# Optimization experiments

Hardware: AMD Instinct MI355X
Metric: run time of the kernel (lower is better)

The kernel has to match this reference:

```python
import jax, jax.numpy as jnp
import numpy as np


def setup_inputs() -> dict:
    key = jax.random.key(0)
    k1, k2, k3, k4, k5 = jax.random.split(key, 5)
    B, S, IN, OUT, GS = 64, 1, 8192, 28672, 128
    n_groups = IN // GS  # 64
    return {
        "input": jax.random.normal(k1, (B, S, IN), dtype=jnp.float32),
        # packed int4 weights: two 4-bit values per byte along in_features
        "qweight": jax.random.randint(k2, (IN // 2, OUT), 0, 256, dtype=jnp.int32),
        # per-group scales (small positive, typical of quantized weights)
        "scales": (jax.random.uniform(k3, (n_groups, OUT), dtype=jnp.float32) * 0.01 + 1e-3),
        # per-group zero points, 4-bit range
        "qzeros": jax.random.randint(k4, (n_groups, OUT), 0, 16, dtype=jnp.int32),
        "bias": jax.random.normal(k5, (OUT,), dtype=jnp.float32),
        "group_size": GS,
    }


def _dequant_int4(qweight, scales, qzeros, group_size):
    # qweight: [in/2, out] bytes; low nibble = even k, high nibble = odd k
    half_in, out_f = qweight.shape
    in_f = half_in * 2
    lo = qweight & 0xF
    hi = (qweight >> 4) & 0xF
    # interleave nibbles along in_features -> [in, out]
    w_q = jnp.stack([lo, hi], axis=1).reshape(in_f, out_f).astype(scales.dtype)
    n_groups = scales.shape[0]
    # (q - zero) * scale, per group of `group_size` rows
    w = (w_q.reshape(n_groups, group_size, out_f)
         - qzeros.astype(scales.dtype)[:, None, :]) * scales[:, None, :]
    return w.reshape(in_f, out_f)


def reference(input, qweight, scales, qzeros, bias, group_size):
    # Fused dequant-int4 matmul (decode path, seq_len == 1): y = x @ W + b
    w = _dequant_int4(qweight, scales, qzeros, group_size)  # [in, out]
    return jnp.einsum('bsi,io->bso', input, w) + bias
```

## Files before the change

### kernel.cpp

```cpp
#include <hip/hip_runtime.h>
#include <hip/hip_bf16.h>


typedef float  f32x4 __attribute__((ext_vector_type(4)));
typedef short  s16x8 __attribute__((ext_vector_type(8)));
typedef int    i32x4 __attribute__((ext_vector_type(4)));

#define K_DIM  8192
#define N_DIM  28672
#define BN     64
#define CK     128
#define NCHUNK 64

__device__ s16x8 g_wsa[NCHUNK * 1024];

__device__ f32x4 llvm_amdgcn_raw_buffer_load_v4f32(i32x4 srsrc, int voff, int soff, int aux) __asm("llvm.amdgcn.raw.buffer.load.v4f32");

static __device__ __forceinline__ short f2bf(float f) {
    return (short)__builtin_bit_cast(unsigned short, __float2bfloat16(f));
}
static __device__ __forceinline__ i32x4 make_srsrc(const void* p, unsigned bytes) {
    union { struct { const void* ptr; unsigned rec; unsigned cfg; } s; i32x4 v; } u;
    u.s.ptr = p; u.s.rec = bytes; u.s.cfg = 0x00020000;
    return u.v;
}

__global__ __launch_bounds__(256)
void prep_a_kernel(const float* __restrict__ x) {
    const int tid = threadIdx.x;
    const int c   = blockIdx.x >> 2;
    const int mb  = blockIdx.x & 3;
    const int k8  = tid & 15;
    const int m   = mb * 16 + (tid >> 4);
    const float* src = x + (size_t)m * K_DIM + c * CK + k8 * 8;
    f32x4 a = *(const f32x4*)src;
    f32x4 b = *(const f32x4*)(src + 4);
    s16x8 o;
    o[0] = f2bf(a[0]); o[1] = f2bf(a[1]); o[2] = f2bf(a[2]); o[3] = f2bf(a[3]);
    o[4] = f2bf(b[0]); o[5] = f2bf(b[1]); o[6] = f2bf(b[2]); o[7] = f2bf(b[3]);
    g_wsa[(size_t)c * 1024 + k8 * 64 + m] = o;
}

__global__ __launch_bounds__(512, 4)
void int4gemm_kernel(const int*   __restrict__ qw,
                     const float* __restrict__ sc,
                     const int*   __restrict__ qz,
                     const float* __restrict__ bias,
                     float*       __restrict__ out)
{
    __shared__ s16x8 lB[2][16 * 64];

    const int tid   = threadIdx.x;
    const int lane  = tid & 63;
    const int w     = tid >> 6;
    const int nbase = blockIdx.x * BN;

    const int col  = lane;
    const int*   qcol = qw + nbase + col;
    const float* scol = sc + nbase + col;
    const int*   zcol = qz + nbase + col;

    const int l15 = lane & 15;
    const int lk  = lane >> 4;
    const int mh  = w >> 2;
    const int wn  = (w & 3) * 16;

    const i32x4 srA  = make_srsrc((const void*)g_wsa, NCHUNK * 1024 * 16);
    const int   voffA = (lk * 64 + mh * 32 + l15) * 16;

    f32x4 acc[2];
    acc[0] = (f32x4)0.0f;
    acc[1] = (f32x4)0.0f;

    int   bvC[8], bvB[8], bvN[8];
    float sC, sB_, sN_;
    int   zC, zB_, zN_;

#pragma unroll
    for (int u = 0; u < 8; ++u) {
        bvC[u] = qcol[(size_t)(8 * w + u) * N_DIM];
        bvB[u] = qcol[(size_t)(64 + 8 * w + u) * N_DIM];
    }
    sC  = scol[0];               zC  = zcol[0];
    sB_ = scol[N_DIM];           zB_ = zcol[N_DIM];

#pragma unroll 2
    for (int c = 0; c < NCHUNK; ++c) {
        f32x4 af[8];
#pragma unroll
        for (int ks = 0; ks < 4; ++ks)
#pragma unroll
            for (int mi = 0; mi < 2; ++mi)
                af[ks * 2 + mi] = llvm_amdgcn_raw_buffer_load_v4f32(
                    srA, voffA + mi * 256, c * 16384 + ks * 4096, 0);
        __builtin_amdgcn_sched_barrier(0);

        const int cb = (c + 2) & (NCHUNK - 1);
#pragma unroll
        for (int u = 0; u < 8; ++u)
            bvN[u] = qcol[(size_t)(cb * 64 + 8 * w + u) * N_DIM];
        sN_ = scol[(size_t)cb * N_DIM];
        zN_ = zcol[(size_t)cb * N_DIM];
        __builtin_amdgcn_sched_barrier(0);

        const float s = sC;
        const float o = -(float)zC * s;
        s16x8 c0, c1;
#pragma unroll
        for (int uu = 0; uu < 4; ++uu) {
            const int v0 = bvC[uu];
            const int v1 = bvC[4 + uu];
            c0[2 * uu]     = f2bf(fmaf((float)(v0 & 15), s, o));
            c0[2 * uu + 1] = f2bf(fmaf((float)(v0 >> 4), s, o));
            c1[2 * uu]     = f2bf(fmaf((float)(v1 & 15), s, o));
            c1[2 * uu + 1] = f2bf(fmaf((float)(v1 >> 4), s, o));
        }
        lB[c & 1][(2 * w) * 64 + col]     = c0;
        lB[c & 1][(2 * w + 1) * 64 + col] = c1;

        asm volatile("s_waitcnt lgkmcnt(0)" ::: "memory");
        asm volatile("s_barrier" ::: "memory");

#pragma unroll
        for (int ks = 0; ks < 4; ++ks) {
            const s16x8 bfr = lB[c & 1][(ks * 4 + lk) * 64 + wn + l15];
            const s16x8 a0  = __builtin_bit_cast(s16x8, af[ks * 2 + 0]);
            const s16x8 a1  = __builtin_bit_cast(s16x8, af[ks * 2 + 1]);
            acc[0] = __builtin_amdgcn_mfma_f32_16x16x32_bf16(a0, bfr, acc[0], 0, 0, 0);
            acc[1] = __builtin_amdgcn_mfma_f32_16x16x32_bf16(a1, bfr, acc[1], 0, 0, 0);
        }

#pragma unroll
        for (int u = 0; u < 8; ++u) { bvC[u] = bvB[u]; bvB[u] = bvN[u]; }
        sC = sB_; sB_ = sN_;
        zC = zB_; zB_ = zN_;
    }

    const int   ncol = nbase + wn + l15;
    const float bv   = bias[ncol];
#pragma unroll
    for (int mi = 0; mi < 2; ++mi) {
#pragma unroll
        for (int j = 0; j < 4; ++j) {
            const int m = mh * 32 + mi * 16 + lk * 4 + j;
            out[(size_t)m * N_DIM + ncol] = acc[mi][j] + bv;
        }
    }
}

extern "C" void kernel_launch(void* const* d_in, const int* in_sizes, int n_in,
                              void* d_out, int out_size, void* d_ws, size_t ws_size,
                              hipStream_t stream) {
    const float* x    = (const float*)d_in[0];
    const int*   qw   = (const int*)d_in[1];
    const float* sc   = (const float*)d_in[2];
    const int*   qz   = (const int*)d_in[3];
    const float* bias = (const float*)d_in[4];
    float*       out  = (float*)d_out;

    prep_a_kernel<<<dim3(256), dim3(256), 0, stream>>>(x);
    int4gemm_kernel<<<dim3(N_DIM / BN), dim3(512), 0, stream>>>(qw, sc, qz, bias, out);
}
```

Measured before the change: 146.7 us.

## Switch to 32x32x16 MFMA with 256-thread blocks and paired-column weight loads

Measured after the change: 129.9 us. -11.4%, faster.

```diff
diff --git a/kernel.cpp b/kernel.cpp
--- a/kernel.cpp
+++ b/kernel.cpp
@@ -2,15 +2,19 @@
 #include <hip/hip_bf16.h>
 
 
-typedef float  f32x4 __attribute__((ext_vector_type(4)));
-typedef short  s16x8 __attribute__((ext_vector_type(8)));
-typedef int    i32x4 __attribute__((ext_vector_type(4)));
+typedef float  f32x2  __attribute__((ext_vector_type(2)));
+typedef float  f32x4  __attribute__((ext_vector_type(4)));
+typedef float  f32x16 __attribute__((ext_vector_type(16)));
+typedef short  s16x8  __attribute__((ext_vector_type(8)));
+typedef int    i32x2  __attribute__((ext_vector_type(2)));
+typedef int    i32x4  __attribute__((ext_vector_type(4)));
 
 #define K_DIM  8192
 #define N_DIM  28672
 #define BN     64
 #define CK     128
 #define NCHUNK 64
+#define NB     (N_DIM / BN)
 
 __device__ s16x8 g_wsa[NCHUNK * 1024];
 
@@ -41,7 +45,7 @@
     g_wsa[(size_t)c * 1024 + k8 * 64 + m] = o;
 }
 
-__global__ __launch_bounds__(512, 4)
+__global__ __launch_bounds__(256, 3)
 void int4gemm_kernel(const int*   __restrict__ qw,
                      const float* __restrict__ sc,
                      const int*   __restrict__ qz,
@@ -55,96 +59,97 @@
     const int w     = tid >> 6;
     const int nbase = blockIdx.x * BN;
 
-    const int col  = lane;
-    const int*   qcol = qw + nbase + col;
-    const float* scol = sc + nbase + col;
-    const int*   zcol = qz + nbase + col;
+    const int p  = tid & 31;
+    const int q  = tid >> 5;
+    const int j0 = nbase + 2 * p;
 
-    const int l15 = lane & 15;
-    const int lk  = lane >> 4;
-    const int mh  = w >> 2;
-    const int wn  = (w & 3) * 16;
+    const int l31 = lane & 31;
+    const int lh  = lane >> 5;
+    const int tm  = w >> 1;
+    const int tn  = w & 1;
 
-    const i32x4 srA  = make_srsrc((const void*)g_wsa, NCHUNK * 1024 * 16);
-    const int   voffA = (lk * 64 + mh * 32 + l15) * 16;
+    const i32x4 srA   = make_srsrc((const void*)g_wsa, NCHUNK * 1024 * 16);
+    const int   voffA = lh * 1024 + (tm * 32 + l31) * 16;
 
-    f32x4 acc[2];
-    acc[0] = (f32x4)0.0f;
-    acc[1] = (f32x4)0.0f;
+    const int*   qbase = qw + j0;
+    const float* scp   = sc + j0;
+    const int*   qzp   = qz + j0;
 
-    int   bvC[8], bvB[8], bvN[8];
-    float sC, sB_, sN_;
-    int   zC, zB_, zN_;
+    f32x16 acc = (f32x16)0.0f;
+
+    i32x2 bvC[8], bvN[8];
+    f32x2 sC, sN;
+    i32x2 zC, zN;
 
 #pragma unroll
-    for (int u = 0; u < 8; ++u) {
-        bvC[u] = qcol[(size_t)(8 * w + u) * N_DIM];
-        bvB[u] = qcol[(size_t)(64 + 8 * w + u) * N_DIM];
-    }
-    sC  = scol[0];               zC  = zcol[0];
-    sB_ = scol[N_DIM];           zB_ = zcol[N_DIM];
+    for (int o2 = 0; o2 < 2; ++o2)
+#pragma unroll
+        for (int r = 0; r < 4; ++r)
+            bvC[o2 * 4 + r] = *(const i32x2*)(qbase + (size_t)((q + 8 * o2) * 4 + r) * N_DIM);
+    sC = *(const f32x2*)scp;
+    zC = *(const i32x2*)qzp;
 
 #pragma unroll 2
     for (int c = 0; c < NCHUNK; ++c) {
         f32x4 af[8];
 #pragma unroll
-        for (int ks = 0; ks < 4; ++ks)
-#pragma unroll
-            for (int mi = 0; mi < 2; ++mi)
-                af[ks * 2 + mi] = llvm_amdgcn_raw_buffer_load_v4f32(
-                    srA, voffA + mi * 256, c * 16384 + ks * 4096, 0);
+        for (int ks = 0; ks < 8; ++ks)
+            af[ks] = llvm_amdgcn_raw_buffer_load_v4f32(srA, voffA,
+                                                       c * 16384 + ks * 2048, 0);
         __builtin_amdgcn_sched_barrier(0);
 
-        const int cb = (c + 2) & (NCHUNK - 1);
+        const int cn = (c + 1) & (NCHUNK - 1);
 #pragma unroll
-        for (int u = 0; u < 8; ++u)
-            bvN[u] = qcol[(size_t)(cb * 64 + 8 * w + u) * N_DIM];
-        sN_ = scol[(size_t)cb * N_DIM];
-        zN_ = zcol[(size_t)cb * N_DIM];
+        for (int o2 = 0; o2 < 2; ++o2)
+#pragma unroll
+            for (int r = 0; r < 4; ++r)
+                bvN[o2 * 4 + r] = *(const i32x2*)(qbase +
+                    (size_t)(cn * 64 + (q + 8 * o2) * 4 + r) * N_DIM);
+        sN = *(const f32x2*)(scp + (size_t)cn * N_DIM);
+        zN = *(const i32x2*)(qzp + (size_t)cn * N_DIM);
         __builtin_amdgcn_sched_barrier(0);
 
-        const float s = sC;
-        const float o = -(float)zC * s;
-        s16x8 c0, c1;
+        const float s0 = sC.x, s1 = sC.y;
+        const float o0 = -(float)zC.x * s0;
+        const float o1 = -(float)zC.y * s1;
 #pragma unroll
-        for (int uu = 0; uu < 4; ++uu) {
-            const int v0 = bvC[uu];
-            const int v1 = bvC[4 + uu];
-            c0[2 * uu]     = f2bf(fmaf((float)(v0 & 15), s, o));
-            c0[2 * uu + 1] = f2bf(fmaf((float)(v0 >> 4), s, o));
-            c1[2 * uu]     = f2bf(fmaf((float)(v1 & 15), s, o));
-            c1[2 * uu + 1] = f2bf(fmaf((float)(v1 >> 4), s, o));
+        for (int o2 = 0; o2 < 2; ++o2) {
+            s16x8 c0, c1;
+#pragma unroll
+            for (int r = 0; r < 4; ++r) {
+                const int vx = bvC[o2 * 4 + r].x;
+                const int vy = bvC[o2 * 4 + r].y;
+                c0[2 * r]     = f2bf(fmaf((float)(vx & 15), s0, o0));
+                c0[2 * r + 1] = f2bf(fmaf((float)(vx >> 4), s0, o0));
+                c1[2 * r]     = f2bf(fmaf((float)(vy & 15), s1, o1));
+                c1[2 * r + 1] = f2bf(fmaf((float)(vy >> 4), s1, o1));
+            }
+            lB[c & 1][(q + 8 * o2) * 64 + 2 * p]     = c0;
+            lB[c & 1][(q + 8 * o2) * 64 + 2 * p + 1] = c1;
         }
-        lB[c & 1][(2 * w) * 64 + col]     = c0;
-        lB[c & 1][(2 * w + 1) * 64 + col] = c1;
 
         asm volatile("s_waitcnt lgkmcnt(0)" ::: "memory");
-        asm volatile("s_barrier" ::: "memory");
+        __builtin_amdgcn_s_barrier();
 
 #pragma unroll
-        for (int ks = 0; ks < 4; ++ks) {
-            const s16x8 bfr = lB[c & 1][(ks * 4 + lk) * 64 + wn + l15];
-            const s16x8 a0  = __builtin_bit_cast(s16x8, af[ks * 2 + 0]);
-            const s16x8 a1  = __builtin_bit_cast(s16x8, af[ks * 2 + 1]);
-            acc[0] = __builtin_amdgcn_mfma_f32_16x16x32_bf16(a0, bfr, acc[0], 0, 0, 0);
-            acc[1] = __builtin_amdgcn_mfma_f32_16x16x32_bf16(a1, bfr, acc[1], 0, 0, 0);
+        for (int ks = 0; ks < 8; ++ks) {
+            const s16x8 bfr = lB[c & 1][(2 * ks + lh) * 64 + tn * 32 + l31];
+            const s16x8 a   = __builtin_bit_cast(s16x8, af[ks]);
+            acc = __builtin_amdgcn_mfma_f32_32x32x16_bf16(a, bfr, acc, 0, 0, 0);
         }
 
 #pragma unroll
-        for (int u = 0; u < 8; ++u) { bvC[u] = bvB[u]; bvB[u] = bvN[u]; }
-        sC = sB_; sB_ = sN_;
-        zC = zB_; zB_ = zN_;
+        for (int u = 0; u < 8; ++u) bvC[u] = bvN[u];
+        sC = sN;
+        zC = zN;
     }
 
-    const int   ncol = nbase + wn + l15;
+    const int   ncol = nbase + tn * 32 + l31;
     const float bv   = bias[ncol];
 #pragma unroll
-    for (int mi = 0; mi < 2; ++mi) {
-#pragma unroll
-        for (int j = 0; j < 4; ++j) {
-            const int m = mh * 32 + mi * 16 + lk * 4 + j;
-            out[(size_t)m * N_DIM + ncol] = acc[mi][j] + bv;
-        }
+    for (int reg = 0; reg < 16; ++reg) {
+        const int m = tm * 32 + (reg & 3) + 8 * (reg >> 2) + 4 * lh;
+        out[(size_t)m * N_DIM + ncol] = acc[reg] + bv;
     }
 }
 
@@ -159,5 +164,5 @@
     float*       out  = (float*)d_out;
 
     prep_a_kernel<<<dim3(256), dim3(256), 0, stream>>>(x);
-    int4gemm_kernel<<<dim3(N_DIM / BN), dim3(512), 0, stream>>>(qw, sc, qz, bias, out);
+    int4gemm_kernel<<<dim3(NB), dim3(256), 0, stream>>>(qw, sc, qz, bias, out);
 }
```
